# Performance work log

Measured on AMD Instinct MI355X. Metric: run time of the kernel, lower is better.

The kernel has to match this reference:

```python
import jax, jax.numpy as jnp
import numpy as np

N = 50000          # number of points
C = 64             # num_clusters (embedding width)
K_RAD = 32         # radius graph max_num_neighbors
K_KNN = 10         # knn graph k


def setup_inputs() -> dict:
    key = jax.random.key(0)
    ks = jax.random.split(key, 8)
    x0 = jax.random.normal(ks[0], (N, 3), jnp.float32)
    pos0 = jax.random.normal(ks[1], (N, 3), jnp.float32)
    # R0/t0 come from rigid_fitting in the original (external helper); use
    # orthonormal matrices from batched QR as realistic per-point rotations.
    A = jax.random.normal(ks[2], (N, 3, 3), jnp.float32)
    R0, _ = jnp.linalg.qr(A)
    t0 = jax.random.normal(ks[3], (N, 3), jnp.float32) * 0.1
    # pool1 k=1 assignment: point i -> cluster assign01[i]
    assign01 = jax.random.randint(ks[4], (N,), 0, C, dtype=jnp.int32)
    # radius graph edges (source, target): each point has K_RAD neighbors
    radius_src = jax.random.randint(ks[5], (N * K_RAD,), 0, N, dtype=jnp.int32)
    radius_dst = jnp.repeat(jnp.arange(N, dtype=jnp.int32), K_RAD)
    # knn-10 graph edges used by WeightedAvg
    knn_src = jax.random.randint(ks[6], (N * K_KNN,), 0, N, dtype=jnp.int32)
    knn_dst = jnp.repeat(jnp.arange(N, dtype=jnp.int32), K_KNN)
    return dict(x0=x0, pos0=pos0, R0=R0, t0=t0, assign01=assign01,
                radius_src=radius_src, radius_dst=radius_dst,
                knn_src=knn_src, knn_dst=knn_dst)


def _rigid_layer(xfeat, pos0, x0, R0, t0, src, dst):
    # RigidPropModule.message + max aggregation (nn=None, lin1: w=-1, b=0.01)
    Ri = R0[dst]                     # [E,3,3] target-side rotation
    ti = t0[dst]                     # [E,3]
    posj = pos0[src]                 # [E,3]
    xj = x0[src]                     # [E,3]
    pred = jnp.einsum('eij,ej->ei', Ri, posj) + ti
    d = jnp.sum((pred - xj) ** 2, axis=-1, keepdims=True)   # [E,1]
    w = jax.nn.sigmoid(-d + 0.01)
    msg = w * xfeat[src]             # [E,C]
    agg = jax.ops.segment_max(msg, dst, num_segments=xfeat.shape[0])
    # messages are non-negative; nodes with no edges get 0 (torch_scatter fill)
    return jnp.maximum(agg, 0.0)


def reference(x0, pos0, R0, t0, assign01, radius_src, radius_dst, knn_src, knn_dst):
    n = x0.shape[0]
    # scatter_add of one-hot cluster embeddings back to points
    emb = jnp.zeros((n, C), jnp.float32).at[jnp.arange(n), assign01].add(1.0)
    m1 = _rigid_layer(emb, pos0, x0, R0, t0, radius_src, radius_dst)
    m2 = _rigid_layer(m1, pos0, x0, R0, t0, radius_src, radius_dst)
    m3 = _rigid_layer(m2, pos0, x0, R0, t0, radius_src, radius_dst)
    m4 = _rigid_layer(m2, pos0, x0, R0, t0, radius_src, radius_dst)
    m5 = _rigid_layer(m2, pos0, x0, R0, t0, radius_src, radius_dst)
    msg = jnp.stack([m1.sum(-1), m2.sum(-1), m3.sum(-1),
                     m4.sum(-1), m5.sum(-1)], axis=-1)      # [N,5]
    # predictor: Linear(5,1) with w=ones, b=-17, then sigmoid
    conf = jax.nn.sigmoid(msg.sum(-1, keepdims=True) - 17.0)  # [N,1]
    # WeightedAvg over knn edges: out[t] = sum_s conf[s]*val[s] / sum_s conf[s]
    cw = conf[knn_src]                                       # [E,1]
    num_R = jax.ops.segment_sum(cw * R0.reshape(n, 9)[knn_src], knn_dst, num_segments=n)
    num_t = jax.ops.segment_sum(cw * t0[knn_src], knn_dst, num_segments=n)
    den = jax.ops.segment_sum(cw, knn_dst, num_segments=n) + 1e-8
    R_out = (num_R / den).reshape(n, 3, 3)
    t_out = num_t / den
    x_out = jnp.einsum('nij,nj->ni', R_out, pos0) + t_out
    return x_out, R_out, t_out
```

## Files before the change

### kernel.cpp

```cpp
#include <hip/hip_runtime.h>
#include <hip/hip_fp16.h>
#include <math.h>

#define N_PTS 50000
#define C_DIM 64
#define K_RAD 32
#define K_KNN 10
#define E_RAD (N_PTS * K_RAD)

__device__ inline __half2 hmax2(__half2 a, __half2 b) {
    __half2 d;
    asm("v_pk_max_f16 %0, %1, %2" : "=v"(d) : "v"(a), "v"(b));
    return d;
}

__device__ inline __half2 shfl_xor_h2(__half2 v, int mask) {
    int i = *(int*)&v;
    int r = __shfl_xor(i, mask);
    return *(__half2*)&r;
}

__global__ void pack_tables_kernel(const float* __restrict__ pos0,
                                   const float* __restrict__ x0,
                                   const int* __restrict__ assign,
                                   const float* __restrict__ R0,
                                   const float* __restrict__ t0,
                                   float4* __restrict__ geo,
                                   float4* __restrict__ rt) {
    int i = blockIdx.x * blockDim.x + threadIdx.x;
    if (i >= N_PTS) return;
    float4 g0 = make_float4(pos0[3 * i], pos0[3 * i + 1], pos0[3 * i + 2], x0[3 * i]);
    float4 g1 = make_float4(x0[3 * i + 1], x0[3 * i + 2], __int_as_float(assign[i]), 0.0f);
    geo[i * 2 + 0] = g0;
    geo[i * 2 + 1] = g1;
    const float* R = R0 + 9 * i;
    rt[i * 3 + 0] = make_float4(R[0], R[1], R[2], R[3]);
    rt[i * 3 + 1] = make_float4(R[4], R[5], R[6], R[7]);
    rt[i * 3 + 2] = make_float4(R[8], t0[3 * i], t0[3 * i + 1], t0[3 * i + 2]);
}

__global__ void ew_layer1_kernel(const float4* __restrict__ geo,
                                 const float* __restrict__ R0,
                                 const float* __restrict__ t0,
                                 const int* __restrict__ src,
                                 unsigned int* __restrict__ packed,
                                 __half* __restrict__ m1,
                                 float* __restrict__ sum1) {
    __shared__ int lm[4][C_DIM];
    int wave = (blockIdx.x * blockDim.x + threadIdx.x) >> 6;
    int lane = threadIdx.x & 63;
    int wslot = threadIdx.x >> 6;
    lm[wslot][lane] = 0;
    int nb = __builtin_amdgcn_readfirstlane(wave);
    float w = 0.0f;
    int a = 0;
    if (lane < 32) {
        int s = src[nb * K_RAD + lane];
        float4 g0 = geo[s * 2 + 0];
        float4 g1 = geo[s * 2 + 1];
        a = __float_as_int(g1.z);
        const float* R = R0 + nb * 9;
        const float* T = t0 + nb * 3;
        float r0 = R[0] * g0.x + R[1] * g0.y + R[2] * g0.z + T[0] - g0.w;
        float r1 = R[3] * g0.x + R[4] * g0.y + R[5] * g0.z + T[1] - g1.x;
        float r2 = R[6] * g0.x + R[7] * g0.y + R[8] * g0.z + T[2] - g1.y;
        float dsq = r0 * r0 + r1 * r1 + r2 * r2;
        w = 1.0f / (1.0f + __expf(dsq - 0.01f));
        unsigned int wb = (unsigned int)__half_as_ushort(__float2half_rn(w));
        packed[nb * K_RAD + lane] = ((unsigned int)s << 16) | wb;
    }
    __syncthreads();
    if (lane < 32) atomicMax(&lm[wslot][a], __float_as_int(w));
    __syncthreads();
    float m = __int_as_float(lm[wslot][lane]);
    if (lane < 32) {
        float lo = __int_as_float(lm[wslot][2 * lane]);
        float hi = __int_as_float(lm[wslot][2 * lane + 1]);
        *(__half2*)(m1 + wave * C_DIM + 2 * lane) = __floats2half2_rn(lo, hi);
    }
    float ssum = m;
#pragma unroll
    for (int off = 32; off > 0; off >>= 1) ssum += __shfl_down(ssum, off);
    if (lane == 0) sum1[wave] = ssum;
}

__global__ void layer_pk_kernel(const unsigned int* __restrict__ packed,
                                const __half* __restrict__ xin,
                                __half* __restrict__ xout,
                                float* __restrict__ sum_out) {
    int wave = (blockIdx.x * blockDim.x + threadIdx.x) >> 6;
    int lane = threadIdx.x & 63;
    if (wave >= N_PTS) return;
    int eslot = lane >> 3;
    int cpos = lane & 7;
    const unsigned int* pkrow = packed + wave * K_RAD;
    __half2 a0 = __float2half2_rn(0.0f), a1 = a0, a2 = a0, a3 = a0;
#pragma unroll
    for (int p = 0; p < 4; ++p) {
        unsigned int pe = pkrow[p * 8 + eslot];
        float4 f = *(const float4*)(xin + (pe >> 16) * C_DIM + cpos * 8);
        __half2* h = (__half2*)&f;
        __half2 w2 = __half2half2(__ushort_as_half((unsigned short)(pe & 0xffffu)));
        a0 = hmax2(a0, __hmul2(w2, h[0]));
        a1 = hmax2(a1, __hmul2(w2, h[1]));
        a2 = hmax2(a2, __hmul2(w2, h[2]));
        a3 = hmax2(a3, __hmul2(w2, h[3]));
    }
#pragma unroll
    for (int off = 8; off < 64; off <<= 1) {
        a0 = hmax2(a0, shfl_xor_h2(a0, off));
        a1 = hmax2(a1, shfl_xor_h2(a1, off));
        a2 = hmax2(a2, shfl_xor_h2(a2, off));
        a3 = hmax2(a3, shfl_xor_h2(a3, off));
    }
    if (eslot == 0) {
        float4 o;
        __half2* oh = (__half2*)&o;
        oh[0] = a0; oh[1] = a1; oh[2] = a2; oh[3] = a3;
        ((float4*)(xout + wave * C_DIM))[cpos] = o;
    }
    float2 v0 = __half22float2(a0), v1 = __half22float2(a1);
    float2 v2 = __half22float2(a2), v3 = __half22float2(a3);
    float s = v0.x + v0.y + v1.x + v1.y + v2.x + v2.y + v3.x + v3.y;
#pragma unroll
    for (int off = 1; off < 8; off <<= 1) s += __shfl_xor(s, off);
    if (lane == 0) sum_out[wave] = s;
}

__global__ void layer3_conf_pk_kernel(const unsigned int* __restrict__ packed,
                                      const __half* __restrict__ xin,
                                      const float* __restrict__ sum1,
                                      const float* __restrict__ sum2,
                                      float* __restrict__ conf) {
    int wave = (blockIdx.x * blockDim.x + threadIdx.x) >> 6;
    int lane = threadIdx.x & 63;
    if (wave >= N_PTS) return;
    int eslot = lane >> 3;
    int cpos = lane & 7;
    const unsigned int* pkrow = packed + wave * K_RAD;
    __half2 a0 = __float2half2_rn(0.0f), a1 = a0, a2 = a0, a3 = a0;
#pragma unroll
    for (int p = 0; p < 4; ++p) {
        unsigned int pe = pkrow[p * 8 + eslot];
        float4 f = *(const float4*)(xin + (pe >> 16) * C_DIM + cpos * 8);
        __half2* h = (__half2*)&f;
        __half2 w2 = __half2half2(__ushort_as_half((unsigned short)(pe & 0xffffu)));
        a0 = hmax2(a0, __hmul2(w2, h[0]));
        a1 = hmax2(a1, __hmul2(w2, h[1]));
        a2 = hmax2(a2, __hmul2(w2, h[2]));
        a3 = hmax2(a3, __hmul2(w2, h[3]));
    }
#pragma unroll
    for (int off = 8; off < 64; off <<= 1) {
        a0 = hmax2(a0, shfl_xor_h2(a0, off));
        a1 = hmax2(a1, shfl_xor_h2(a1, off));
        a2 = hmax2(a2, shfl_xor_h2(a2, off));
        a3 = hmax2(a3, shfl_xor_h2(a3, off));
    }
    float2 v0 = __half22float2(a0), v1 = __half22float2(a1);
    float2 v2 = __half22float2(a2), v3 = __half22float2(a3);
    float s = v0.x + v0.y + v1.x + v1.y + v2.x + v2.y + v3.x + v3.y;
#pragma unroll
    for (int off = 1; off < 8; off <<= 1) s += __shfl_xor(s, off);
    if (lane == 0) {
        float tot = sum1[wave] + sum2[wave] + 3.0f * s - 17.0f;
        conf[wave] = 1.0f / (1.0f + __expf(-tot));
    }
}

__global__ void wavg_kernel(const int* __restrict__ knn_src,
                            const float* __restrict__ conf,
                            const float4* __restrict__ rt,
                            const float* __restrict__ pos0,
                            float* __restrict__ out) {
    int t = blockIdx.x * blockDim.x + threadIdx.x;
    if (t >= N_PTS) return;
    float nR[9] = {0, 0, 0, 0, 0, 0, 0, 0, 0};
    float nt0 = 0.0f, nt1 = 0.0f, nt2 = 0.0f;
    float den = 1e-8f;
    for (int j = 0; j < K_KNN; ++j) {
        int s = knn_src[t * K_KNN + j];
        float c = conf[s];
        float4 q0 = rt[s * 3 + 0];
        float4 q1 = rt[s * 3 + 1];
        float4 q2 = rt[s * 3 + 2];
        nR[0] += c * q0.x; nR[1] += c * q0.y; nR[2] += c * q0.z; nR[3] += c * q0.w;
        nR[4] += c * q1.x; nR[5] += c * q1.y; nR[6] += c * q1.z; nR[7] += c * q1.w;
        nR[8] += c * q2.x;
        nt0 += c * q2.y; nt1 += c * q2.z; nt2 += c * q2.w;
        den += c;
    }
    float inv = 1.0f / den;
    float Ro[9];
#pragma unroll
    for (int k = 0; k < 9; ++k) Ro[k] = nR[k] * inv;
    float to0 = nt0 * inv, to1 = nt1 * inv, to2 = nt2 * inv;
    float px = pos0[t * 3 + 0], py = pos0[t * 3 + 1], pz = pos0[t * 3 + 2];
    out[t * 3 + 0] = Ro[0] * px + Ro[1] * py + Ro[2] * pz + to0;
    out[t * 3 + 1] = Ro[3] * px + Ro[4] * py + Ro[5] * pz + to1;
    out[t * 3 + 2] = Ro[6] * px + Ro[7] * py + Ro[8] * pz + to2;
    float* Rout = out + N_PTS * 3;
#pragma unroll
    for (int k = 0; k < 9; ++k) Rout[t * 9 + k] = Ro[k];
    float* tout = out + N_PTS * 3 + N_PTS * 9;
    tout[t * 3 + 0] = to0;
    tout[t * 3 + 1] = to1;
    tout[t * 3 + 2] = to2;
}

extern "C" void kernel_launch(void* const* d_in, const int* in_sizes, int n_in,
                              void* d_out, int out_size, void* d_ws, size_t ws_size,
                              hipStream_t stream) {
    const float* x0 = (const float*)d_in[0];
    const float* pos0 = (const float*)d_in[1];
    const float* R0 = (const float*)d_in[2];
    const float* t0 = (const float*)d_in[3];
    const int* assign01 = (const int*)d_in[4];
    const int* radius_src = (const int*)d_in[5];
    const int* knn_src = (const int*)d_in[7];

    char* ws = (char*)d_ws;
    unsigned int* packed = (unsigned int*)ws;
    __half* mA = (__half*)(ws + 6400000);
    __half* mB = (__half*)(ws + 12800000);
    float4* geo = (float4*)(ws + 19200000);
    float4* rt = (float4*)(ws + 20800000);
    float* sum1 = (float*)(ws + 23200000);
    float* sum2 = (float*)(ws + 23400000);
    float* conf = (float*)(ws + 23600000);
    float* out = (float*)d_out;

    int layer_blocks = (N_PTS * 64 + 255) / 256;

    pack_tables_kernel<<<(N_PTS + 255) / 256, 256, 0, stream>>>(
        pos0, x0, assign01, R0, t0, geo, rt);

    ew_layer1_kernel<<<layer_blocks, 256, 0, stream>>>(
        geo, R0, t0, radius_src, packed, mA, sum1);

    layer_pk_kernel<<<layer_blocks, 256, 0, stream>>>(
        packed, mA, mB, sum2);

    layer3_conf_pk_kernel<<<layer_blocks, 256, 0, stream>>>(
        packed, mB, sum1, sum2, conf);

    wavg_kernel<<<(N_PTS + 255) / 256, 256, 0, stream>>>(
        knn_src, conf, rt, pos0, out);
}
```

Before: 140.8 us.

## Pack conf into padded RT table and split gathers across lane groups

Confidence is now written into a padding slot of a 64-byte-per-point R/t table. The weighted-average kernel uses four lanes per point, each gathering one float4, so each neighbour's conf arrives with its rotation and translation rather than as a separate scattered load. Layer 1 splits each edge's 32-byte geometry gather across two lanes and exchanges halves with shuffles. The max-layer kernels read their packed edge entries with one 16-byte load per lane instead of four scalar loads. In exchange the table grows, the output step needs extra cross-lane shuffles, and the weighted-average kernel leaves one lane in four idle during output.

Measured after the change: 141.0 us. About the same (+0.1%).

```diff
diff --git a/kernel.cpp b/kernel.cpp
--- a/kernel.cpp
+++ b/kernel.cpp
@@ -26,17 +26,15 @@
                                    const float* __restrict__ R0,
                                    const float* __restrict__ t0,
                                    float4* __restrict__ geo,
-                                   float4* __restrict__ rt) {
+                                   float4* __restrict__ rt4) {
     int i = blockIdx.x * blockDim.x + threadIdx.x;
     if (i >= N_PTS) return;
-    float4 g0 = make_float4(pos0[3 * i], pos0[3 * i + 1], pos0[3 * i + 2], x0[3 * i]);
-    float4 g1 = make_float4(x0[3 * i + 1], x0[3 * i + 2], __int_as_float(assign[i]), 0.0f);
-    geo[i * 2 + 0] = g0;
-    geo[i * 2 + 1] = g1;
+    geo[i * 2 + 0] = make_float4(pos0[3 * i], pos0[3 * i + 1], pos0[3 * i + 2], x0[3 * i]);
+    geo[i * 2 + 1] = make_float4(x0[3 * i + 1], x0[3 * i + 2], __int_as_float(assign[i]), 0.0f);
     const float* R = R0 + 9 * i;
-    rt[i * 3 + 0] = make_float4(R[0], R[1], R[2], R[3]);
-    rt[i * 3 + 1] = make_float4(R[4], R[5], R[6], R[7]);
-    rt[i * 3 + 2] = make_float4(R[8], t0[3 * i], t0[3 * i + 1], t0[3 * i + 2]);
+    rt4[i * 4 + 0] = make_float4(R[0], R[1], R[2], R[3]);
+    rt4[i * 4 + 1] = make_float4(R[4], R[5], R[6], R[7]);
+    rt4[i * 4 + 2] = make_float4(R[8], t0[3 * i], t0[3 * i + 1], t0[3 * i + 2]);
 }
 
 __global__ void ew_layer1_kernel(const float4* __restrict__ geo,
@@ -52,25 +50,26 @@
     int wslot = threadIdx.x >> 6;
     lm[wslot][lane] = 0;
     int nb = __builtin_amdgcn_readfirstlane(wave);
-    float w = 0.0f;
-    int a = 0;
-    if (lane < 32) {
-        int s = src[nb * K_RAD + lane];
-        float4 g0 = geo[s * 2 + 0];
-        float4 g1 = geo[s * 2 + 1];
-        a = __float_as_int(g1.z);
+    int e = lane >> 1;
+    int part = lane & 1;
+    int s = src[nb * K_RAD + e];
+    float4 g = geo[s * 2 + part];
+    float ox = __shfl_xor(g.x, 1);
+    float oy = __shfl_xor(g.y, 1);
+    float oz = __shfl_xor(g.z, 1);
+    __syncthreads();
+    if (part == 0) {
         const float* R = R0 + nb * 9;
         const float* T = t0 + nb * 3;
-        float r0 = R[0] * g0.x + R[1] * g0.y + R[2] * g0.z + T[0] - g0.w;
-        float r1 = R[3] * g0.x + R[4] * g0.y + R[5] * g0.z + T[1] - g1.x;
-        float r2 = R[6] * g0.x + R[7] * g0.y + R[8] * g0.z + T[2] - g1.y;
+        float r0 = R[0] * g.x + R[1] * g.y + R[2] * g.z + T[0] - g.w;
+        float r1 = R[3] * g.x + R[4] * g.y + R[5] * g.z + T[1] - ox;
+        float r2 = R[6] * g.x + R[7] * g.y + R[8] * g.z + T[2] - oy;
         float dsq = r0 * r0 + r1 * r1 + r2 * r2;
-        w = 1.0f / (1.0f + __expf(dsq - 0.01f));
+        float w = 1.0f / (1.0f + __expf(dsq - 0.01f));
         unsigned int wb = (unsigned int)__half_as_ushort(__float2half_rn(w));
-        packed[nb * K_RAD + lane] = ((unsigned int)s << 16) | wb;
-    }
-    __syncthreads();
-    if (lane < 32) atomicMax(&lm[wslot][a], __float_as_int(w));
+        packed[nb * K_RAD + e] = ((unsigned int)s << 16) | wb;
+        atomicMax(&lm[wslot][__float_as_int(oz)], __float_as_int(w));
+    }
     __syncthreads();
     float m = __int_as_float(lm[wslot][lane]);
     if (lane < 32) {
@@ -93,11 +92,12 @@
     if (wave >= N_PTS) return;
     int eslot = lane >> 3;
     int cpos = lane & 7;
-    const unsigned int* pkrow = packed + wave * K_RAD;
+    uint4 pv = ((const uint4*)(packed + wave * K_RAD))[eslot];
+    unsigned int pes[4] = {pv.x, pv.y, pv.z, pv.w};
     __half2 a0 = __float2half2_rn(0.0f), a1 = a0, a2 = a0, a3 = a0;
 #pragma unroll
     for (int p = 0; p < 4; ++p) {
-        unsigned int pe = pkrow[p * 8 + eslot];
+        unsigned int pe = pes[p];
         float4 f = *(const float4*)(xin + (pe >> 16) * C_DIM + cpos * 8);
         __half2* h = (__half2*)&f;
         __half2 w2 = __half2half2(__ushort_as_half((unsigned short)(pe & 0xffffu)));
@@ -131,17 +131,18 @@
                                       const __half* __restrict__ xin,
                                       const float* __restrict__ sum1,
                                       const float* __restrict__ sum2,
-                                      float* __restrict__ conf) {
+                                      float* __restrict__ rt4f) {
     int wave = (blockIdx.x * blockDim.x + threadIdx.x) >> 6;
     int lane = threadIdx.x & 63;
     if (wave >= N_PTS) return;
     int eslot = lane >> 3;
     int cpos = lane & 7;
-    const unsigned int* pkrow = packed + wave * K_RAD;
+    uint4 pv = ((const uint4*)(packed + wave * K_RAD))[eslot];
+    unsigned int pes[4] = {pv.x, pv.y, pv.z, pv.w};
     __half2 a0 = __float2half2_rn(0.0f), a1 = a0, a2 = a0, a3 = a0;
 #pragma unroll
     for (int p = 0; p < 4; ++p) {
-        unsigned int pe = pkrow[p * 8 + eslot];
+        unsigned int pe = pes[p];
         float4 f = *(const float4*)(xin + (pe >> 16) * C_DIM + cpos * 8);
         __half2* h = (__half2*)&f;
         __half2 w2 = __half2half2(__ushort_as_half((unsigned short)(pe & 0xffffu)));
@@ -164,48 +165,56 @@
     for (int off = 1; off < 8; off <<= 1) s += __shfl_xor(s, off);
     if (lane == 0) {
         float tot = sum1[wave] + sum2[wave] + 3.0f * s - 17.0f;
-        conf[wave] = 1.0f / (1.0f + __expf(-tot));
+        rt4f[wave * 16 + 12] = 1.0f / (1.0f + __expf(-tot));
     }
 }
 
 __global__ void wavg_kernel(const int* __restrict__ knn_src,
-                            const float* __restrict__ conf,
-                            const float4* __restrict__ rt,
+                            const float4* __restrict__ rt4,
                             const float* __restrict__ pos0,
                             float* __restrict__ out) {
-    int t = blockIdx.x * blockDim.x + threadIdx.x;
+    int gid = blockIdx.x * blockDim.x + threadIdx.x;
+    int lane = gid & 63;
+    int t = (gid >> 6) * 16 + (lane >> 2);
+    int part = lane & 3;
     if (t >= N_PTS) return;
-    float nR[9] = {0, 0, 0, 0, 0, 0, 0, 0, 0};
-    float nt0 = 0.0f, nt1 = 0.0f, nt2 = 0.0f;
-    float den = 1e-8f;
+    float4 acc = make_float4(0.f, 0.f, 0.f, 0.f);
     for (int j = 0; j < K_KNN; ++j) {
         int s = knn_src[t * K_KNN + j];
-        float c = conf[s];
-        float4 q0 = rt[s * 3 + 0];
-        float4 q1 = rt[s * 3 + 1];
-        float4 q2 = rt[s * 3 + 2];
-        nR[0] += c * q0.x; nR[1] += c * q0.y; nR[2] += c * q0.z; nR[3] += c * q0.w;
-        nR[4] += c * q1.x; nR[5] += c * q1.y; nR[6] += c * q1.z; nR[7] += c * q1.w;
-        nR[8] += c * q2.x;
-        nt0 += c * q2.y; nt1 += c * q2.z; nt2 += c * q2.w;
-        den += c;
-    }
+        float4 q = rt4[s * 4 + part];
+        float c = __shfl(q.x, lane | 3);
+        if (part == 3) {
+            acc.x += c;
+        } else {
+            acc.x += c * q.x; acc.y += c * q.y;
+            acc.z += c * q.z; acc.w += c * q.w;
+        }
+    }
+    float den = __shfl(acc.x, lane | 3) + 1e-8f;
     float inv = 1.0f / den;
-    float Ro[9];
-#pragma unroll
-    for (int k = 0; k < 9; ++k) Ro[k] = nR[k] * inv;
-    float to0 = nt0 * inv, to1 = nt1 * inv, to2 = nt2 * inv;
+    float4 sc = make_float4(acc.x * inv, acc.y * inv, acc.z * inv, acc.w * inv);
+    int base = lane & ~3;
+    float R3 = __shfl(sc.w, base + 0);
+    float R6 = __shfl(sc.z, base + 1);
+    float R7 = __shfl(sc.w, base + 1);
+    float t0v = __shfl(sc.y, base + 2);
+    float t1v = __shfl(sc.z, base + 2);
     float px = pos0[t * 3 + 0], py = pos0[t * 3 + 1], pz = pos0[t * 3 + 2];
-    out[t * 3 + 0] = Ro[0] * px + Ro[1] * py + Ro[2] * pz + to0;
-    out[t * 3 + 1] = Ro[3] * px + Ro[4] * py + Ro[5] * pz + to1;
-    out[t * 3 + 2] = Ro[6] * px + Ro[7] * py + Ro[8] * pz + to2;
     float* Rout = out + N_PTS * 3;
-#pragma unroll
-    for (int k = 0; k < 9; ++k) Rout[t * 9 + k] = Ro[k];
-    float* tout = out + N_PTS * 3 + N_PTS * 9;
-    tout[t * 3 + 0] = to0;
-    tout[t * 3 + 1] = to1;
-    tout[t * 3 + 2] = to2;
+    float* tout = out + N_PTS * 12;
+    if (part == 0) {
+        out[t * 3 + 0] = sc.x * px + sc.y * py + sc.z * pz + t0v;
+        Rout[t * 9 + 0] = sc.x; Rout[t * 9 + 1] = sc.y;
+        Rout[t * 9 + 2] = sc.z; Rout[t * 9 + 3] = sc.w;
+    } else if (part == 1) {
+        out[t * 3 + 1] = R3 * px + sc.x * py + sc.y * pz + t1v;
+        Rout[t * 9 + 4] = sc.x; Rout[t * 9 + 5] = sc.y;
+        Rout[t * 9 + 6] = sc.z; Rout[t * 9 + 7] = sc.w;
+    } else if (part == 2) {
+        out[t * 3 + 2] = R6 * px + R7 * py + sc.x * pz + sc.w;
+        Rout[t * 9 + 8] = sc.x;
+        tout[t * 3 + 0] = sc.y; tout[t * 3 + 1] = sc.z; tout[t * 3 + 2] = sc.w;
+    }
 }
 
 extern "C" void kernel_launch(void* const* d_in, const int* in_sizes, int n_in,
@@ -224,16 +233,15 @@
     __half* mA = (__half*)(ws + 6400000);
     __half* mB = (__half*)(ws + 12800000);
     float4* geo = (float4*)(ws + 19200000);
-    float4* rt = (float4*)(ws + 20800000);
-    float* sum1 = (float*)(ws + 23200000);
-    float* sum2 = (float*)(ws + 23400000);
-    float* conf = (float*)(ws + 23600000);
+    float4* rt4 = (float4*)(ws + 20800000);
+    float* sum1 = (float*)(ws + 24000000);
+    float* sum2 = (float*)(ws + 24200000);
     float* out = (float*)d_out;
 
     int layer_blocks = (N_PTS * 64 + 255) / 256;
 
     pack_tables_kernel<<<(N_PTS + 255) / 256, 256, 0, stream>>>(
-        pos0, x0, assign01, R0, t0, geo, rt);
+        pos0, x0, assign01, R0, t0, geo, rt4);
 
     ew_layer1_kernel<<<layer_blocks, 256, 0, stream>>>(
         geo, R0, t0, radius_src, packed, mA, sum1);
@@ -242,8 +250,8 @@
         packed, mA, mB, sum2);
 
     layer3_conf_pk_kernel<<<layer_blocks, 256, 0, stream>>>(
-        packed, mB, sum1, sum2, conf);
-
-    wavg_kernel<<<(N_PTS + 255) / 256, 256, 0, stream>>>(
-        knn_src, conf, rt, pos0, out);
-}
+        packed, mB, sum1, sum2, (float*)rt4);
+
+    wavg_kernel<<<(N_PTS * 4 + 255) / 256, 256, 0, stream>>>(
+        knn_src, rt4, pos0, out);
+}
```
